# Performance work log

Measured on AMD Instinct MI355X. Metric: run time of the kernel, lower is better.

The kernel has to match this reference:

```python
import jax, jax.numpy as jnp
import numpy as np

B = 2048          # number of graphs in the batch
ACT_DIM = 14      # nodes per graph (act_dim)
C = 128           # in_channels
H = 256           # hidden_size


def _pair_edges(n):
    ii, jj = np.meshgrid(np.arange(n), np.arange(n), indexing='ij')
    m = ii != jj
    return np.stack([ii[m], jj[m]], axis=1)  # [n*(n-1), 2]


def setup_inputs() -> dict:
    key = jax.random.key(0)
    ks = jax.random.split(key, 12)
    edges_np = _pair_edges(ACT_DIM)                       # [182, 2]
    offs = (np.arange(B) * ACT_DIM)[:, None, None]
    batched = (edges_np[None] + offs).reshape(-1, 2)      # [B*182, 2]
    edge_index = jnp.asarray(batched.T, dtype=jnp.int64 if jax.config.jax_enable_x64 else jnp.int32)
    edges = jnp.asarray(edges_np, dtype=jnp.int32)

    def lin(k, o, i):
        return jax.random.normal(k, (o, i), jnp.float32) * (1.0 / np.sqrt(i))

    return {
        'state': jax.random.normal(ks[0], (B * ACT_DIM, C), jnp.float32),
        'conv_w': lin(ks[1], C, C),
        'conv_b': jnp.zeros((C,), jnp.float32),
        'lin1_w': lin(ks[2], H, 2 * C),
        'lin1_b': jax.random.normal(ks[3], (H,), jnp.float32) * 0.01,
        'lin2_w': lin(ks[4], H, H),
        'lin2_b': jax.random.normal(ks[5], (H,), jnp.float32) * 0.01,
        'mu_w': lin(ks[6], 1, H),
        'mu_b': jnp.zeros((1,), jnp.float32),
        'sig_w': lin(ks[7], 1, H),
        'sig_b': jnp.zeros((1,), jnp.float32),
        'noise': jax.random.normal(ks[8], (B, edges_np.shape[0]), jnp.float32),
        'edge_index': edge_index,
        'edges': edges,
    }


def _gcn_conv(x, edge_index, w, b):
    # Standard GCNConv: add self-loops, symmetric normalization, x @ W^T, scatter-add, + bias.
    n = x.shape[0]
    loops = jnp.arange(n, dtype=edge_index.dtype)
    src = jnp.concatenate([edge_index[0], loops])
    dst = jnp.concatenate([edge_index[1], loops])
    deg = jax.ops.segment_sum(jnp.ones_like(src, dtype=x.dtype), dst, num_segments=n)
    dinv = jax.lax.rsqrt(deg)  # deg >= 1 because of self-loops
    norm = dinv[src] * dinv[dst]                       # [E+N]
    xw = x @ w.T                                       # [N, C]
    msg = xw[src] * norm[:, None]                      # gather + scale
    return jax.ops.segment_sum(msg, dst, num_segments=n) + b


def reference(state, conv_w, conv_b, lin1_w, lin1_b, lin2_w, lin2_b,
              mu_w, mu_b, sig_w, sig_b, noise, edge_index, edges):
    out = jax.nn.relu(_gcn_conv(state, edge_index, conv_w, conv_b))
    x = (out + state).reshape(-1, ACT_DIM, C)          # [B, 14, C]
    es, ed = edges[:, 0], edges[:, 1]
    ef = jnp.concatenate([x[:, es, :], x[:, ed, :]], axis=2)   # [B, E, 2C]
    h = jax.nn.leaky_relu(jnp.einsum('bec,hc->beh', ef, lin1_w) + lin1_b)
    h = jax.nn.leaky_relu(jnp.einsum('beh,gh->beg', h, lin2_w) + lin2_b)
    mu = jax.nn.softplus(jnp.einsum('beh,oh->beo', h, mu_w) + mu_b)[..., 0]   # [B, E]
    std = jax.nn.softplus(jnp.einsum('beh,oh->beo', h, sig_w) + sig_b)[..., 0]
    action = mu + std * noise                          # Normal rsample with fixed eps
    log_prob = jnp.sum(
        -0.5 * ((action - mu) / std) ** 2 - jnp.log(std) - 0.5 * jnp.log(2.0 * jnp.pi),
        axis=-1)                                       # [B]
    return action, log_prob
```

## Files before the change

### kernel.cpp

```cpp
#include <hip/hip_runtime.h>

#define ACT 14
#define CC 128
#define HH 256
#define EPB 182
#define NB 2048
#define M2 (NB*EPB)
#define NS 520
#define LP_CONST (-182.0f * 0.91893853320467274f)

typedef short s16x8 __attribute__((ext_vector_type(8)));
typedef _Float16 h16x8 __attribute__((ext_vector_type(8)));
typedef _Float16 h16x2 __attribute__((ext_vector_type(2)));
typedef float f32x2 __attribute__((ext_vector_type(2)));
typedef float f32x4 __attribute__((ext_vector_type(4)));
typedef int   i32x4 __attribute__((ext_vector_type(4)));
typedef float f32x16 __attribute__((ext_vector_type(16)));

__device__ __forceinline__ float softplusf(float x) { return x > 15.f ? x : log1pf(expf(x)); }
__device__ __forceinline__ float leaky(float x) { return fmaxf(x, 0.01f * x); }

__device__ __forceinline__ short f2bf(float f) {
    unsigned u = __float_as_uint(f);
    unsigned r = (u + 0x7fffu + ((u >> 16) & 1u)) >> 16;
    return (short)r;
}
__device__ __forceinline__ float bflo(int m) { return __uint_as_float(((unsigned)m) << 16); }
__device__ __forceinline__ float bfhi(int m) { return __uint_as_float((unsigned)m & 0xffff0000u); }

__device__ __forceinline__ short f2h(float f) {
    _Float16 h = (_Float16)f;
    return __builtin_bit_cast(short, h);
}
__device__ __forceinline__ int pk_f16(float a, float b) {
    return __builtin_bit_cast(int, __builtin_amdgcn_cvt_pkrtz(a, b));
}
__device__ __forceinline__ int pk_f16_rn(float a, float b) {
    return (int)(unsigned short)f2h(a) | ((int)f2h(b) << 16);
}
__device__ __forceinline__ float fdot2i(int a, int b, float c) {
#if __has_builtin(__builtin_amdgcn_fdot2)
    return __builtin_amdgcn_fdot2(__builtin_bit_cast(h16x2, a),
                                  __builtin_bit_cast(h16x2, b), c, false);
#else
    h16x2 av = __builtin_bit_cast(h16x2, a), bv = __builtin_bit_cast(h16x2, b);
    return c + (float)av[0] * (float)bv[0] + (float)av[1] * (float)bv[1];
#endif
}

__global__ __launch_bounds__(256) void prep_kernel(
    const float* __restrict__ conv_w, const float* __restrict__ lin1_w,
    const float* __restrict__ lin2_w, const float* __restrict__ mu_w,
    const float* __restrict__ sig_w,
    short* __restrict__ W2h, short* __restrict__ W1h,
    int* __restrict__ cwPT, int* __restrict__ w1sPT,
    int* __restrict__ msbf)
{
    int i = blockIdx.x * 256 + threadIdx.x;
    W2h[i] = f2h(lin2_w[i]);
    {
        int n = i >> 7, k = i & 127;
        float v = (n < 256) ? lin1_w[n * 256 + k] : lin1_w[(n - 256) * 256 + 128 + k];
        W1h[i] = f2h(v);
    }
    if (i < 8192) {
        int j = i >> 6, p = i & 63;
        cwPT[i] = pk_f16_rn(conv_w[j * 128 + 2 * p], conv_w[j * 128 + 2 * p + 1]);
    }
    if (i < 16384) {
        int h = i >> 6, p = i & 63;
        float a0 = lin1_w[h * 256 + 2 * p]     + lin1_w[h * 256 + 128 + 2 * p];
        float a1 = lin1_w[h * 256 + 2 * p + 1] + lin1_w[h * 256 + 128 + 2 * p + 1];
        w1sPT[i] = pk_f16_rn(a0, a1);
    }
    if (i < 256) msbf[i] = (int)(unsigned short)f2bf(mu_w[i]) | ((int)f2bf(sig_w[i]) << 16);
}

__global__ __launch_bounds__(512, 4) void actor_kernel(
    const float* __restrict__ state, const short* __restrict__ W1h,
    const short* __restrict__ W2h,
    const int* __restrict__ cwPT, const float* __restrict__ conv_b,
    const int* __restrict__ w1sPT, const float* __restrict__ lin1_b,
    const float* __restrict__ lin2_b, const int* __restrict__ msbf,
    const float* __restrict__ mu_b, const float* __restrict__ sig_b,
    const float* __restrict__ noise, const int* __restrict__ edges,
    float* __restrict__ out)
{
    __shared__ short h1L[2][8192];
    __shared__ short nodeL[2 * ACT * NS];
    __shared__ int   ssP[2][64];
    __shared__ int   gP[2][64];
    __shared__ float wL[2][256];
    __shared__ float b2L[256];
    __shared__ int   msL[256];
    __shared__ int2  edgeL[192];
    __shared__ float mu_acc[384], sg_acc[384];
    __shared__ float lp_acc[2];

    short* stateL = &h1L[0][0];

    const int t = threadIdx.x, b = blockIdx.x;
    const int lane = t & 63, ln = lane & 15, q = lane >> 4;
    const int w = t >> 6;
    const int l32 = lane & 31, hf = lane >> 5;

    #pragma unroll
    for (int it = 0; it < 2; ++it) {
        int idx = it * 512 + t;
        int bt = idx >> 9, row = (idx >> 5) & 15, c4 = idx & 31;
        int kk = c4 >> 3, k8 = (c4 & 7) * 4;
        int* dst = (int*)&stateL[bt * 2560 + kk * 640 + row * 40 + k8];
        if (row < ACT) {
            f32x4 x = *(const f32x4*)(state + ((size_t)(2 * b + bt) * ACT + row) * CC + c4 * 4);
            dst[0] = pk_f16(x[0], x[1]); dst[1] = pk_f16(x[2], x[3]);
        } else { dst[0] = 0; dst[1] = 0; }
    }
    if (t < 256) {
        b2L[t] = lin2_b[t];
        msL[t] = msbf[t];
    } else {
        int i = t - 256, bt = i >> 7, c = i & 127;
        const float* sp = state + (size_t)(2 * b + bt) * ACT * CC + c;
        float s = 0.f;
        #pragma unroll
        for (int r = 0; r < ACT; ++r) s += sp[r * CC];
        s *= (1.f / 14.f);
        float s2 = __shfl_xor(s, 1);
        if (!(c & 1)) ssP[bt][c >> 1] = pk_f16(s, s2);
    }
    if (t < EPB) edgeL[t] = ((const int2*)edges)[t];
    if (t < 384) { mu_acc[t] = 0.f; sg_acc[t] = 0.f; }
    if (t < 2) lp_acc[t] = 0.f;
    __syncthreads();

    {
        int bt = t >> 8, r = t & 255, j = r >> 1, s = r & 1;
        const i32x4* wp = (const i32x4*)&cwPT[j * 64 + s * 32];
        const i32x4* sp4 = (const i32x4*)&ssP[bt][s * 32];
        float a0 = 0.f, a1 = 0.f, a2 = 0.f, a3 = 0.f;
        #pragma unroll
        for (int u = 0; u < 8; ++u) {
            i32x4 wv = wp[u]; i32x4 sv = sp4[u];
            a0 = fdot2i(wv[0], sv[0], a0); a1 = fdot2i(wv[1], sv[1], a1);
            a2 = fdot2i(wv[2], sv[2], a2); a3 = fdot2i(wv[3], sv[3], a3);
        }
        float a = (a0 + a1) + (a2 + a3);
        a += __shfl_xor(a, 1);
        float gf = fmaxf(a + conv_b[j], 0.f);
        float go = __shfl_xor(gf, 2);
        if ((r & 3) == 0) gP[bt][r >> 2] = pk_f16(gf, go);
    }
    __syncthreads();
    {
        int bt = t >> 8, h = t & 255;
        const i32x4* wp = (const i32x4*)&w1sPT[h * 64];
        const i32x4* gp4 = (const i32x4*)&gP[bt][0];
        float a0 = 0.f, a1 = 0.f, a2 = 0.f, a3 = 0.f;
        #pragma unroll 8
        for (int u = 0; u < 16; ++u) {
            i32x4 wv = wp[u]; i32x4 gv = gp4[u];
            a0 = fdot2i(wv[0], gv[0], a0); a1 = fdot2i(wv[1], gv[1], a1);
            a2 = fdot2i(wv[2], gv[2], a2); a3 = fdot2i(wv[3], gv[3], a3);
        }
        wL[bt][h] = (a0 + a1) + (a2 + a3) + lin1_b[h];
    }
    __syncthreads();

    f32x4 zero4 = {0.f, 0.f, 0.f, 0.f};
    f32x4 nacc[2][4];
    #pragma unroll
    for (int bt = 0; bt < 2; ++bt) {
        nacc[bt][0] = zero4; nacc[bt][1] = zero4;
        nacc[bt][2] = zero4; nacc[bt][3] = zero4;
    }
    #pragma unroll
    for (int c = 0; c < 4; ++c) {
        h16x8 a80 = __builtin_bit_cast(h16x8, *(const s16x8*)&stateL[0 * 2560 + c * 640 + ln * 40 + q * 8]);
        h16x8 a81 = __builtin_bit_cast(h16x8, *(const s16x8*)&stateL[1 * 2560 + c * 640 + ln * 40 + q * 8]);
        #pragma unroll
        for (int i = 0; i < 4; ++i) {
            int ct = w + 8 * i;
            h16x8 b8 = __builtin_bit_cast(h16x8, *(const s16x8*)&W1h[(size_t)(ct * 16 + ln) * CC + c * 32 + q * 8]);
            nacc[0][i] = __builtin_amdgcn_mfma_f32_16x16x32_f16(a80, b8, nacc[0][i], 0, 0, 0);
            nacc[1][i] = __builtin_amdgcn_mfma_f32_16x16x32_f16(a81, b8, nacc[1][i], 0, 0, 0);
        }
    }

    s16x8 wa[16];
    #pragma unroll
    for (int c = 0; c < 16; ++c)
        wa[c] = *(const s16x8*)&W2h[(size_t)(w * 32 + l32) * HH + c * 16 + hf * 8];

    #pragma unroll
    for (int bt = 0; bt < 2; ++bt)
        #pragma unroll
        for (int i = 0; i < 4; ++i) {
            int col = (w + 8 * i) * 16 + ln;
            float wadd = (col < HH) ? wL[bt][col] : 0.f;
            #pragma unroll
            for (int rg = 0; rg < 4; ++rg) {
                int node = q * 4 + rg;
                if (node < ACT) nodeL[(bt * ACT + node) * NS + col] = f2h(nacc[bt][i][rg] + wadd);
            }
        }
    __syncthreads();

    const h16x2 c001 = {(_Float16)0.01f, (_Float16)0.01f};
    auto build = [&](int tile, int bufi) {
        int bt = (tile >= 6) ? 1 : 0;
        int e32 = t & 31;
        int e = (tile - bt * 6) * 32 + e32;
        bool ok = e < EPB;
        int2 p = edgeL[ok ? e : 0];
        int base = bt * ACT * NS;
        int uo = base + p.x * NS, vo = base + HH + p.y * NS;
        int sl = t >> 5;
        #pragma unroll
        for (int s = 0; s < 2; ++s) {
            int slot = sl + 16 * s;
            int chunk = slot >> 1, half = slot & 1;
            int koff = chunk * 16 + half * 8;
            int o[4] = {0, 0, 0, 0};
            if (ok) {
                s16x8 u8 = *(const s16x8*)&nodeL[uo + koff];
                s16x8 v8 = *(const s16x8*)&nodeL[vo + koff];
                const int* ui = (const int*)&u8;
                const int* vi = (const int*)&v8;
                #pragma unroll
                for (int j = 0; j < 4; ++j) {
                    h16x2 uu = __builtin_bit_cast(h16x2, ui[j]);
                    h16x2 vv = __builtin_bit_cast(h16x2, vi[j]);
                    h16x2 sum = uu + vv;
                    h16x2 lk  = __builtin_elementwise_max(sum, sum * c001);
                    o[j] = __builtin_bit_cast(int, lk);
                }
            }
            *(s16x8*)&h1L[bufi][chunk * 512 + (half * 32 + e32) * 8] = *(const s16x8*)o;
        }
    };

    build(0, 0);
    for (int tile = 0; tile < 12; ++tile) {
        __syncthreads();
        if (tile < 11) build(tile + 1, (tile + 1) & 1);
        const int buf = tile & 1;
        f32x16 acc;
        #pragma unroll
        for (int r = 0; r < 16; ++r) acc[r] = 0.f;
        #pragma unroll
        for (int c = 0; c < 16; ++c) {
            h16x8 b8 = __builtin_bit_cast(h16x8, *(const s16x8*)&h1L[buf][c * 512 + lane * 8]);
            h16x8 a8 = __builtin_bit_cast(h16x8, wa[c]);
            acc = __builtin_amdgcn_mfma_f32_32x32x16_f16(a8, b8, acc, 0, 0, 0);
        }
        int bt = (tile >= 6) ? 1 : 0;
        int col0 = (tile - bt * 6) * 32;
        float pmu = 0.f, psg = 0.f;
        const int nsb = w * 32 + 4 * hf;
        #pragma unroll
        for (int g = 0; g < 4; ++g) {
            f32x4 b4 = *(const f32x4*)&b2L[nsb + 8 * g];
            i32x4 m4 = *(const i32x4*)&msL[nsb + 8 * g];
            #pragma unroll
            for (int i = 0; i < 4; ++i) {
                float h2 = leaky(acc[g * 4 + i] + b4[i]);
                pmu += bflo(m4[i]) * h2;
                psg += bfhi(m4[i]) * h2;
            }
        }
        pmu += __shfl_xor(pmu, 32);
        psg += __shfl_xor(psg, 32);
        if (lane < 32) atomicAdd(&mu_acc[bt * 192 + col0 + l32], pmu);
        else           atomicAdd(&sg_acc[bt * 192 + col0 + l32], psg);
    }
    __syncthreads();

    float lpv = 0.f;
    {
        int bt = t >> 8, i = t & 255;
        if (i < EPB) {
            float mu = softplusf(mu_acc[bt * 192 + i] + mu_b[0]);
            float sd = softplusf(sg_acc[bt * 192 + i] + sig_b[0]);
            float z = noise[(size_t)(2 * b + bt) * EPB + i];
            out[(size_t)(2 * b + bt) * EPB + i] = mu + sd * z;
            lpv = -0.5f * z * z - logf(sd);
        }
    }
    #pragma unroll
    for (int off = 1; off < 64; off <<= 1) lpv += __shfl_xor(lpv, off);
    if (lane == 0) atomicAdd(&lp_acc[t >> 8], lpv);
    __syncthreads();
    if (t < 2) out[M2 + 2 * b + t] = lp_acc[t] + LP_CONST;
}

extern "C" void kernel_launch(void* const* d_in, const int* in_sizes, int n_in,
                              void* d_out, int out_size, void* d_ws, size_t ws_size,
                              hipStream_t stream)
{
    const float* state  = (const float*)d_in[0];
    const float* conv_w = (const float*)d_in[1];
    const float* conv_b = (const float*)d_in[2];
    const float* lin1_w = (const float*)d_in[3];
    const float* lin1_b = (const float*)d_in[4];
    const float* lin2_w = (const float*)d_in[5];
    const float* lin2_b = (const float*)d_in[6];
    const float* mu_w   = (const float*)d_in[7];
    const float* mu_b   = (const float*)d_in[8];
    const float* sig_w  = (const float*)d_in[9];
    const float* sig_b  = (const float*)d_in[10];
    const float* noise  = (const float*)d_in[11];
    const int*   edges  = (const int*)d_in[13];
    float* out = (float*)d_out;

    char* ws = (char*)d_ws;
    short* W2h    = (short*)ws;  ws += 65536 * 2;
    short* W1h    = (short*)ws;  ws += 65536 * 2;
    int*   cwPT   = (int*)ws;    ws += 8192 * 4;
    int*   w1sPT  = (int*)ws;    ws += 16384 * 4;
    int*   msbf   = (int*)ws;    ws += 256 * 4;

    prep_kernel<<<256, 256, 0, stream>>>(conv_w, lin1_w, lin2_w, mu_w, sig_w,
                                         W2h, W1h, cwPT, w1sPT, msbf);
    actor_kernel<<<NB / 2, 512, 0, stream>>>(state, W1h, W2h,
                                             cwPT, conv_b, w1sPT, lin1_b,
                                             lin2_b, msbf, mu_b, sig_b,
                                             noise, edges, out);
}
```

Before: 199.3 us.

## Use 16x16x32 MFMA tiles with XOR-swizzled LDS layout for lin2 GEMM

Replaces the 32x32x16 MFMA inner loop for the second linear layer with four 16x16x32 MFMA accumulators per wave. The A fragments from W2 and the h1 tile layout in LDS are reorganised to match. The h1 buffer now uses a row-per-edge layout with an XOR swizzle to avoid bank conflicts, and s_setprio is raised around the MFMA loop. The epilogue reduction is reworked to use two shuffle steps and a four-way atomic split, which adds some shuffle overhead.

```diff
diff --git a/kernel.cpp b/kernel.cpp
--- a/kernel.cpp
+++ b/kernel.cpp
@@ -15,7 +15,6 @@
 typedef float f32x2 __attribute__((ext_vector_type(2)));
 typedef float f32x4 __attribute__((ext_vector_type(4)));
 typedef int   i32x4 __attribute__((ext_vector_type(4)));
-typedef float f32x16 __attribute__((ext_vector_type(16)));
 
 __device__ __forceinline__ float softplusf(float x) { return x > 15.f ? x : log1pf(expf(x)); }
 __device__ __forceinline__ float leaky(float x) { return fmaxf(x, 0.01f * x); }
@@ -102,7 +101,7 @@
     const int t = threadIdx.x, b = blockIdx.x;
     const int lane = t & 63, ln = lane & 15, q = lane >> 4;
     const int w = t >> 6;
-    const int l32 = lane & 31, hf = lane >> 5;
+    const int l32 = lane & 31;
 
     #pragma unroll
     for (int it = 0; it < 2; ++it) {
@@ -186,10 +185,12 @@
         }
     }
 
-    s16x8 wa[16];
-    #pragma unroll
-    for (int c = 0; c < 16; ++c)
-        wa[c] = *(const s16x8*)&W2h[(size_t)(w * 32 + l32) * HH + c * 16 + hf * 8];
+    s16x8 wa16[16];
+    #pragma unroll
+    for (int rf = 0; rf < 2; ++rf)
+        #pragma unroll
+        for (int kf = 0; kf < 8; ++kf)
+            wa16[rf * 8 + kf] = *(const s16x8*)&W2h[(size_t)(w * 32 + rf * 16 + ln) * HH + kf * 32 + q * 8];
 
     #pragma unroll
     for (int bt = 0; bt < 2; ++bt)
@@ -215,11 +216,11 @@
         int base = bt * ACT * NS;
         int uo = base + p.x * NS, vo = base + HH + p.y * NS;
         int sl = t >> 5;
+        char* hb = (char*)&h1L[bufi][0];
+        int wswz = (e32 & 7) << 4;
         #pragma unroll
         for (int s = 0; s < 2; ++s) {
-            int slot = sl + 16 * s;
-            int chunk = slot >> 1, half = slot & 1;
-            int koff = chunk * 16 + half * 8;
+            int koff = (sl + 16 * s) * 8;
             int o[4] = {0, 0, 0, 0};
             if (ok) {
                 s16x8 u8 = *(const s16x8*)&nodeL[uo + koff];
@@ -235,43 +236,62 @@
                     o[j] = __builtin_bit_cast(int, lk);
                 }
             }
-            *(s16x8*)&h1L[bufi][chunk * 512 + (half * 32 + e32) * 8] = *(const s16x8*)o;
+            int byteoff = (e32 << 9) + (((koff << 1)) ^ wswz);
+            *(s16x8*)(hb + byteoff) = *(const s16x8*)o;
         }
     };
+
+    const int qx = q << 4, swz = (ln & 7) << 4, lnb = ln << 9;
 
     build(0, 0);
     for (int tile = 0; tile < 12; ++tile) {
         __syncthreads();
         if (tile < 11) build(tile + 1, (tile + 1) & 1);
         const int buf = tile & 1;
-        f32x16 acc;
-        #pragma unroll
-        for (int r = 0; r < 16; ++r) acc[r] = 0.f;
-        #pragma unroll
-        for (int c = 0; c < 16; ++c) {
-            h16x8 b8 = __builtin_bit_cast(h16x8, *(const s16x8*)&h1L[buf][c * 512 + lane * 8]);
-            h16x8 a8 = __builtin_bit_cast(h16x8, wa[c]);
-            acc = __builtin_amdgcn_mfma_f32_32x32x16_f16(a8, b8, acc, 0, 0, 0);
-        }
+        const char* hb = (const char*)&h1L[buf][0];
+
+        f32x4 acc00 = zero4, acc01 = zero4, acc10 = zero4, acc11 = zero4;
+        __builtin_amdgcn_s_setprio(1);
+        #pragma unroll
+        for (int kf = 0; kf < 8; ++kf) {
+            int off = lnb + (((kf << 6) | qx) ^ swz);
+            h16x8 b0 = __builtin_bit_cast(h16x8, *(const s16x8*)(hb + off));
+            h16x8 b1 = __builtin_bit_cast(h16x8, *(const s16x8*)(hb + off + 8192));
+            h16x8 a0 = __builtin_bit_cast(h16x8, wa16[kf]);
+            h16x8 a1 = __builtin_bit_cast(h16x8, wa16[8 + kf]);
+            acc00 = __builtin_amdgcn_mfma_f32_16x16x32_f16(a0, b0, acc00, 0, 0, 0);
+            acc01 = __builtin_amdgcn_mfma_f32_16x16x32_f16(a0, b1, acc01, 0, 0, 0);
+            acc10 = __builtin_amdgcn_mfma_f32_16x16x32_f16(a1, b0, acc10, 0, 0, 0);
+            acc11 = __builtin_amdgcn_mfma_f32_16x16x32_f16(a1, b1, acc11, 0, 0, 0);
+        }
+        __builtin_amdgcn_s_setprio(0);
+
         int bt = (tile >= 6) ? 1 : 0;
         int col0 = (tile - bt * 6) * 32;
-        float pmu = 0.f, psg = 0.f;
-        const int nsb = w * 32 + 4 * hf;
-        #pragma unroll
-        for (int g = 0; g < 4; ++g) {
-            f32x4 b4 = *(const f32x4*)&b2L[nsb + 8 * g];
-            i32x4 m4 = *(const i32x4*)&msL[nsb + 8 * g];
+        float pmu0 = 0.f, pmu1 = 0.f, psg0 = 0.f, psg1 = 0.f;
+        #pragma unroll
+        for (int rf = 0; rf < 2; ++rf) {
+            int rb = w * 32 + rf * 16 + q * 4;
+            f32x4 b4 = *(const f32x4*)&b2L[rb];
+            i32x4 m4 = *(const i32x4*)&msL[rb];
+            f32x4 a0 = rf ? acc10 : acc00;
+            f32x4 a1 = rf ? acc11 : acc01;
             #pragma unroll
             for (int i = 0; i < 4; ++i) {
-                float h2 = leaky(acc[g * 4 + i] + b4[i]);
-                pmu += bflo(m4[i]) * h2;
-                psg += bfhi(m4[i]) * h2;
+                float h0 = leaky(a0[i] + b4[i]);
+                float h1 = leaky(a1[i] + b4[i]);
+                pmu0 += bflo(m4[i]) * h0;  psg0 += bfhi(m4[i]) * h0;
+                pmu1 += bflo(m4[i]) * h1;  psg1 += bfhi(m4[i]) * h1;
             }
         }
-        pmu += __shfl_xor(pmu, 32);
-        psg += __shfl_xor(psg, 32);
-        if (lane < 32) atomicAdd(&mu_acc[bt * 192 + col0 + l32], pmu);
-        else           atomicAdd(&sg_acc[bt * 192 + col0 + l32], psg);
+        pmu0 += __shfl_xor(pmu0, 16); pmu0 += __shfl_xor(pmu0, 32);
+        pmu1 += __shfl_xor(pmu1, 16); pmu1 += __shfl_xor(pmu1, 32);
+        psg0 += __shfl_xor(psg0, 16); psg0 += __shfl_xor(psg0, 32);
+        psg1 += __shfl_xor(psg1, 16); psg1 += __shfl_xor(psg1, 32);
+        if (q == 0)      atomicAdd(&mu_acc[bt * 192 + col0 + ln],      pmu0);
+        else if (q == 1) atomicAdd(&mu_acc[bt * 192 + col0 + 16 + ln], pmu1);
+        else if (q == 2) atomicAdd(&sg_acc[bt * 192 + col0 + ln],      psg0);
+        else             atomicAdd(&sg_acc[bt * 192 + col0 + 16 + ln], psg1);
     }
     __syncthreads();
 
```

Result: no change. 202.6 us (+1.7%).
